# Performance work log

Hardware: AMD Instinct MI355X
Metric: run time of the kernel (lower is better)

Reference implementation:

```python
import jax, jax.numpy as jnp
import numpy as np

B, SQ, SK = 2, 2048, 2048
D, H = 1024, 16
HD = D // H              # head_dim = 64
R = 128                  # rel_pos_max_distance
P = 2 * R + 1            # num_pos_ids = 257
RADIUS = 256             # local_attention_radius


def setup_inputs() -> dict:
    key = jax.random.key(0)
    ks = jax.random.split(key, 8)
    s = 0.02
    return {
        "Q": jax.random.normal(ks[0], (B, SQ, D), dtype=jnp.float32),
        "K": jax.random.normal(ks[1], (B, SK, D), dtype=jnp.float32),
        "V": jax.random.normal(ks[2], (B, SK, D), dtype=jnp.float32),
        "Wq": jax.random.normal(ks[3], (D, D), dtype=jnp.float32) * s,
        "Wk": jax.random.normal(ks[4], (D, D), dtype=jnp.float32) * s,
        "Wv": jax.random.normal(ks[5], (D, D), dtype=jnp.float32) * s,
        "Wo": jax.random.normal(ks[6], (D, D), dtype=jnp.float32) * s,
        "E": jax.random.normal(ks[7], (P, D), dtype=jnp.float32) * s,  # rel_embeds
    }


def _split_heads(x, W):
    # bias-free projection then split: B x S x D -> B x H x S x HD
    y = x @ W.T
    b, s, _ = y.shape
    return y.reshape(b, s, H, HD).transpose(0, 2, 1, 3)


def reference(Q, K, V, Wq, Wk, Wv, Wo, E):
    q = _split_heads(Q, Wq)  # B,H,Sq,HD
    k = _split_heads(K, Wk)  # B,H,Sk,HD
    v = _split_heads(V, Wv)  # B,H,Sk,HD

    # rel_embeds reshape matches torch: E[p] viewed as (head_dim, num_heads)
    rel = E.reshape(P, HD, H).transpose(2, 0, 1)           # H,P,HD
    Q_rel = jnp.einsum("bhqd,hpd->bhqp", q, rel)           # B,H,Sq,P

    # slided relative position ids: clip(j - i, -R, R) + R
    i = jnp.arange(SQ)[:, None]
    j = jnp.arange(SK)[None, :]
    rel_ids = jnp.clip(j - i, -R, R) + R                   # Sq,Sk
    rel_shift = jnp.take_along_axis(
        Q_rel, jnp.broadcast_to(rel_ids, (B, H, SQ, SK)), axis=3
    )                                                       # B,H,Sq,Sk

    energy = (jnp.einsum("bhqd,bhkd->bhqk", q, k) + rel_shift) / jnp.sqrt(
        jnp.float32(HD)
    )

    # local attention mask: True = masked (outside window of radius RADIUS)
    mask = jnp.abs(j - i) > RADIUS                          # Sq,Sk
    mask = mask & ~jnp.all(mask, axis=-1, keepdims=True)    # never mask full rows
    energy = jnp.where(mask[None, None], -jnp.inf, energy)

    attn = jax.nn.softmax(energy, axis=-1)                  # B,H,Sq,Sk
    out = jnp.einsum("bhqk,bhkd->bhqd", attn, v)            # B,H,Sq,HD
    # torch: view(B,H,Sq,HD).permute(0,2,3,1).flatten(2,3) -> B,Sq,(HD*H)
    out = out.transpose(0, 2, 3, 1).reshape(B, SQ, D)
    return out @ Wo.T
```

## Files before the change

### kernel.cpp

```cpp
#include <hip/hip_runtime.h>
#include <hip/hip_bf16.h>

#define BATCH 2
#define SQn 2048
#define SKn 2048
#define DMODEL 1024
#define NH 16
#define HD 64
#define NPOS 257
#define RWIN 128
#define RADIUS 256

typedef __attribute__((ext_vector_type(8))) short bf16x8;
typedef __attribute__((ext_vector_type(4))) float f32x4;

static __device__ __forceinline__ unsigned short f2bf(float f) {
    union { float f; unsigned u; } v; v.f = f;
    unsigned r = (v.u + 0x7FFFu + ((v.u >> 16) & 1u)) >> 16;
    return (unsigned short)r;
}
static __device__ __forceinline__ float bf2f(unsigned short b) {
    union { unsigned u; float f; } v; v.u = ((unsigned)b) << 16;
    return v.f;
}

static __device__ __forceinline__ void gl_lds16(const unsigned short* g, unsigned short* l) {
    __builtin_amdgcn_global_load_lds(
        (const __attribute__((address_space(1))) unsigned*)g,
        (__attribute__((address_space(3))) unsigned*)l, 16, 0, 0);
}

#define SWZ(row) (((row) ^ ((row) >> 2)) & 3)

__global__ __launch_bounds__(256) void convert_kernel(
    const float* __restrict__ Q, const float* __restrict__ K, const float* __restrict__ V,
    const float* __restrict__ Wq, const float* __restrict__ Wk, const float* __restrict__ Wv,
    const float* __restrict__ Wo,
    unsigned short* __restrict__ xb,
    unsigned short* __restrict__ wb,
    unsigned short* __restrict__ woh)
{
    int i = blockIdx.x * 256 + threadIdx.x;
    if (i < 3145728) {
        int which = i >> 20;
        int off = i & 1048575;
        const float* src = which == 0 ? Q : (which == 1 ? K : V);
        unsigned short* dst = xb + (size_t)which * 4194304;
        float4 v4 = ((const float4*)src)[off];
        ushort4 o4;
        o4.x = f2bf(v4.x); o4.y = f2bf(v4.y); o4.z = f2bf(v4.z); o4.w = f2bf(v4.w);
        ((ushort4*)dst)[off] = o4;
    } else {
        int i2 = i - 3145728;
        int which = i2 >> 18;
        int off = i2 & 262143;
        if (which < 3) {
            const float* src = which == 0 ? Wq : (which == 1 ? Wk : Wv);
            unsigned short* dst = wb + (size_t)which * 1048576;
            float4 v4 = ((const float4*)src)[off];
            ushort4 o4;
            o4.x = f2bf(v4.x); o4.y = f2bf(v4.y); o4.z = f2bf(v4.z); o4.w = f2bf(v4.w);
            ((ushort4*)dst)[off] = o4;
        } else {
            float4 v4 = ((const float4*)Wo)[off];
            int e0 = off * 4;
            int n  = e0 >> 10;
            int c0 = e0 & 1023;
            int d  = c0 >> 4;
            int h0 = c0 & 15;
            woh[((size_t)(h0 + 0) * 1024 + n) * 64 + d] = f2bf(v4.x);
            woh[((size_t)(h0 + 1) * 1024 + n) * 64 + d] = f2bf(v4.y);
            woh[((size_t)(h0 + 2) * 1024 + n) * 64 + d] = f2bf(v4.z);
            woh[((size_t)(h0 + 3) * 1024 + n) * 64 + d] = f2bf(v4.w);
        }
    }
}

__global__ __launch_bounds__(256) void mfma_gemm(
    const unsigned short* __restrict__ Xall,
    const unsigned short* __restrict__ Wall,
    unsigned short* __restrict__ Yall)
{
    __shared__ unsigned short sA[128 * 32];
    __shared__ unsigned short sB[128 * 32];
    __shared__ unsigned short sT[64 * 136];

    const int tid  = threadIdx.x;
    const int wv   = tid >> 6;
    const int lane = tid & 63;
    const int quad = lane >> 4;
    const int l15  = lane & 15;
    const int z    = blockIdx.z;
    const int m0   = blockIdx.x * 128;
    const int n0   = blockIdx.y * 128;
    const int wr   = (wv >> 1) * 64;
    const int wc   = (wv & 1) * 64;

    const unsigned short* X = Xall + (size_t)z * (4096 * 1024);
    const unsigned short* W = Wall + (size_t)z * (1024 * 1024);

    int aoff[4], boff[4];
#pragma unroll
    for (int t = 0; t < 4; ++t) {
        int row = wr + t * 16 + l15;
        aoff[t] = row * 32 + ((quad ^ SWZ(row)) * 8);
        int col = wc + t * 16 + l15;
        boff[t] = col * 32 + ((quad ^ SWZ(col)) * 8);
    }

    int srow[2], scg[2], sf[2];
#pragma unroll
    for (int r = 0; r < 2; ++r) {
        int f = r * 256 + tid;
        sf[r] = f;
        srow[r] = f >> 2;
        scg[r] = (f & 3) ^ SWZ(srow[r]);
    }

    f32x4 acc[4][4];
#pragma unroll
    for (int i = 0; i < 4; ++i)
#pragma unroll
        for (int j = 0; j < 4; ++j)
            acc[i][j] = (f32x4){0.f, 0.f, 0.f, 0.f};

    for (int k0 = 0; k0 < 1024; k0 += 32) {
        __syncthreads();
#pragma unroll
        for (int r = 0; r < 2; ++r) {
            gl_lds16(X + (size_t)(m0 + srow[r]) * 1024 + k0 + scg[r] * 8, &sA[sf[r] * 8]);
            gl_lds16(W + (size_t)(n0 + srow[r]) * 1024 + k0 + scg[r] * 8, &sB[sf[r] * 8]);
        }
        __syncthreads();

        bf16x8 af[4], bfr[4];
#pragma unroll
        for (int t = 0; t < 4; ++t) af[t]  = *(const bf16x8*)&sA[aoff[t]];
#pragma unroll
        for (int t = 0; t < 4; ++t) bfr[t] = *(const bf16x8*)&sB[boff[t]];
#pragma unroll
        for (int i = 0; i < 4; ++i)
#pragma unroll
            for (int j = 0; j < 4; ++j)
                acc[i][j] = __builtin_amdgcn_mfma_f32_16x16x32_bf16(af[i], bfr[j], acc[i][j], 0, 0, 0);
    }

    unsigned short* Y = Yall + (size_t)z * (4096 * 1024);
    const int b_ = m0 >> 11;
    const int s0 = m0 & (SQn - 1);

    if (z < 2) {
#pragma unroll
        for (int i = 0; i < 4; ++i) {
            int mbase = s0 + wr + i * 16 + quad * 4;
#pragma unroll
            for (int j = 0; j < 4; ++j) {
                int col = n0 + wc + j * 16 + l15;
                int h = col >> 6, dd = col & 63;
                unsigned short* yb = Y + (((size_t)(b_ * NH + h) * SQn) << 6) + dd;
#pragma unroll
                for (int r = 0; r < 4; ++r)
                    yb[(size_t)(mbase + r) << 6] = f2bf(acc[i][j][r]);
            }
        }
    } else {
#pragma unroll
        for (int hh = 0; hh < 2; ++hh) {
            __syncthreads();
            if ((wv & 1) == hh) {
#pragma unroll
                for (int i = 0; i < 4; ++i) {
                    int mloc = wr + i * 16 + quad * 4;
#pragma unroll
                    for (int j = 0; j < 4; ++j) {
                        ushort4 pk;
                        pk.x = f2bf(acc[i][j][0]);
                        pk.y = f2bf(acc[i][j][1]);
                        pk.z = f2bf(acc[i][j][2]);
                        pk.w = f2bf(acc[i][j][3]);
                        *(ushort4*)&sT[(j * 16 + l15) * 136 + mloc] = pk;
                    }
                }
            }
            __syncthreads();
            int h = (n0 >> 6) + hh;
            unsigned short* yb = Y + ((size_t)(b_ * NH + h) * HD) * SKn + s0;
#pragma unroll
            for (int it = 0; it < 4; ++it) {
                int u = it * 256 + tid;
                int dd = u >> 4, mc = u & 15;
                uint4 val = *(const uint4*)&sT[dd * 136 + mc * 8];
                *(uint4*)(yb + (size_t)dd * SKn + mc * 8) = val;
            }
        }
    }
}

__global__ __launch_bounds__(256) void gemm_out(
    const unsigned short* __restrict__ aoh,
    const unsigned short* __restrict__ woh,
    float* __restrict__ Y)
{
    __shared__ unsigned short sA[64 * 32];
    __shared__ unsigned short sB[128 * 32];

    const int tid  = threadIdx.x;
    const int wv   = tid >> 6;
    const int lane = tid & 63;
    const int quad = lane >> 4;
    const int l15  = lane & 15;
    const int m0   = blockIdx.x * 64;
    const int n0   = blockIdx.y * 128;
    const int wr   = (wv >> 1) * 32;
    const int wc   = (wv & 1) * 64;
    const int b_   = m0 >> 11;
    const int s0   = m0 & (SQn - 1);

    int aoff[2], boff[4];
#pragma unroll
    for (int i = 0; i < 2; ++i) {
        int row = wr + i * 16 + l15;
        aoff[i] = row * 32 + ((quad ^ SWZ(row)) * 8);
    }
#pragma unroll
    for (int j = 0; j < 4; ++j) {
        int col = wc + j * 16 + l15;
        boff[j] = col * 32 + ((quad ^ SWZ(col)) * 8);
    }

    const int arow = tid >> 2;
    const int acs  = (tid & 3) ^ SWZ(arow);
    int bf_[2], brow[2], bcs[2];
#pragma unroll
    for (int r = 0; r < 2; ++r) {
        int f = r * 256 + tid;
        bf_[r] = f; brow[r] = f >> 2; bcs[r] = (f & 3) ^ SWZ(brow[r]);
    }

    f32x4 acc[2][4];
#pragma unroll
    for (int i = 0; i < 2; ++i)
#pragma unroll
        for (int j = 0; j < 4; ++j)
            acc[i][j] = (f32x4){0.f, 0.f, 0.f, 0.f};

    for (int h = 0; h < NH; ++h) {
        const unsigned short* Ah = aoh + ((size_t)(b_ * NH + h) * SQn + s0) * HD;
        const unsigned short* Bh = woh + ((size_t)h * 1024 + n0) * HD;
#pragma unroll
        for (int k0 = 0; k0 < 64; k0 += 32) {
            __syncthreads();
            gl_lds16(Ah + (size_t)arow * HD + k0 + acs * 8, &sA[tid * 8]);
#pragma unroll
            for (int r = 0; r < 2; ++r)
                gl_lds16(Bh + (size_t)brow[r] * HD + k0 + bcs[r] * 8, &sB[bf_[r] * 8]);
            __syncthreads();

            bf16x8 af[2], bfr[4];
#pragma unroll
            for (int i = 0; i < 2; ++i) af[i]  = *(const bf16x8*)&sA[aoff[i]];
#pragma unroll
            for (int j = 0; j < 4; ++j) bfr[j] = *(const bf16x8*)&sB[boff[j]];
#pragma unroll
            for (int i = 0; i < 2; ++i)
#pragma unroll
                for (int j = 0; j < 4; ++j)
                    acc[i][j] = __builtin_amdgcn_mfma_f32_16x16x32_bf16(af[i], bfr[j], acc[i][j], 0, 0, 0);
        }
    }

#pragma unroll
    for (int i = 0; i < 2; ++i) {
        int mbase = m0 + wr + i * 16 + quad * 4;
#pragma unroll
        for (int j = 0; j < 4; ++j) {
            int col = n0 + wc + j * 16 + l15;
#pragma unroll
            for (int r = 0; r < 4; ++r)
                Y[(size_t)(mbase + r) * DMODEL + col] = acc[i][j][r];
        }
    }
}

__global__ __launch_bounds__(256) void relt_kernel(
    const float* __restrict__ E, unsigned short* __restrict__ relTb)
{
    int idx = blockIdx.x * 256 + threadIdx.x;
    const int total = NH * NPOS * HD;
    if (idx < total) {
        int d = idx & (HD - 1);
        int p = (idx >> 6) % NPOS;
        int h = idx / (NPOS * HD);
        relTb[idx] = f2bf(E[(size_t)p * DMODEL + d * NH + h]);
    }
}

#define BIAS_S 9.765625e-4f

__global__ __launch_bounds__(256, 4) void attn_mfma(
    const unsigned short* __restrict__ q,
    const unsigned short* __restrict__ k,
    const unsigned short* __restrict__ vT,
    const unsigned short* __restrict__ relTb,
    unsigned short* __restrict__ aoh)
{
    __shared__ unsigned short sK[64 * 64];
    __shared__ unsigned short sP[4][16 * 72];
    __shared__ signed char    sq8[64 * 260];
    unsigned short* const sQ = (unsigned short*)sq8;

    const int tid  = threadIdx.x;
    const int w    = tid >> 6;
    const int lane = tid & 63;
    const int quad = lane >> 4;
    const int l15  = lane & 15;
    const int xcd  = blockIdx.x & 7;
    const int sidx = blockIdx.x >> 3;
    const int bh   = (xcd << 2) | (sidx >> 5);
    const int q0   = (sidx & 31) << 6;
    const int h    = bh & (NH - 1);

    const int f1 = tid,       row1 = f1 >> 3;
    const int c1 = ((f1 & 7) ^ (row1 & 7)) * 8;
    const int f2 = 256 + tid, row2 = f2 >> 3;
    const int c2 = ((f2 & 7) ^ (row2 & 7)) * 8;

    {
        const unsigned short* gq = q + ((size_t)bh * SQn + q0) * HD;
        gl_lds16(gq + row1 * HD + c1, &sQ[f1 * 8]);
        gl_lds16(gq + row2 * HD + c2, &sQ[f2 * 8]);
    }
    __syncthreads();

    const int qrow = w * 16 + l15;
    const int qs = (quad ^ (qrow & 7)) * 8;
    bf16x8 a0 = *(const bf16x8*)&sQ[qrow * 64 + qs];
    bf16x8 a1 = *(const bf16x8*)&sQ[qrow * 64 + (qs ^ 32)];

    const int myrow = w * 16 + quad * 4;
    for (int c5 = 0; c5 < 5; ++c5) {
        __syncthreads();
        const unsigned short* gr = relTb + ((size_t)h * NPOS + c5 * 64) * HD;
        gl_lds16(gr + row1 * HD + c1, &sK[f1 * 8]);
        gl_lds16(gr + row2 * HD + c2, &sK[f2 * 8]);
        __syncthreads();
#pragma unroll
        for (int t = 0; t < 4; ++t) {
            int prow = t * 16 + l15;
            int ks = (quad ^ (prow & 7)) * 8;
            bf16x8 b0 = *(const bf16x8*)&sK[prow * 64 + ks];
            bf16x8 b1 = *(const bf16x8*)&sK[prow * 64 + (ks ^ 32)];
            f32x4 cc = {0.f, 0.f, 0.f, 0.f};
            cc = __builtin_amdgcn_mfma_f32_16x16x32_bf16(a0, b0, cc, 0, 0, 0);
            cc = __builtin_amdgcn_mfma_f32_16x16x32_bf16(a1, b1, cc, 0, 0, 0);
            int pos = c5 * 64 + t * 16 + l15;
            if (pos < NPOS) {
#pragma unroll
                for (int r = 0; r < 4; ++r) {
                    int iq = (int)rintf(cc[r] * 128.0f);
                    iq = iq < -127 ? -127 : (iq > 127 ? 127 : iq);
                    sq8[(myrow + r) * 260 + pos] = (signed char)iq;
                }
            }
        }
    }
    __syncthreads();

    float bias0[4], bias256[4];
#pragma unroll
    for (int r = 0; r < 4; ++r) {
        bias0[r]   = (float)sq8[(myrow + r) * 260 + 0]   * BIAS_S;
        bias256[r] = (float)sq8[(myrow + r) * 260 + 256] * BIAS_S;
    }

    const int lo = (q0 - RADIUS) > 0 ? (q0 - RADIUS) : 0;
    const int hi = (q0 + 63 + RADIUS) < (SKn - 1) ? (q0 + 63 + RADIUS) : (SKn - 1);
    const int nt = ((hi - lo) >> 6) + 1;
    const int e_ = l15 - quad * 4;

    const unsigned short* kg = k  + (size_t)bh * SKn * HD;
    const unsigned short* vg = vT + (size_t)bh * HD * SKn;

    float lacc[4] = {0.f, 0.f, 0.f, 0.f};
    f32x4 o[4];
#pragma unroll
    for (int t = 0; t < 4; ++t) o[t] = (f32x4){0.f, 0.f, 0.f, 0.f};

    {
        gl_lds16(kg + (size_t)(lo + row1) * HD + c1, &sK[f1 * 8]);
        gl_lds16(kg + (size_t)(lo + row2) * HD + c2, &sK[f2 * 8]);
    }

    for (int kt = 0; kt < nt; ++kt) {
        const int kb = lo + (kt << 6);
        __syncthreads();

        bf16x8 kf0[4], kf1[4];
#pragma unroll
        for (int t = 0; t < 4; ++t) {
            int prow = t * 16 + l15;
            int ks = (quad ^ (prow & 7)) * 8;
            kf0[t] = *(const bf16x8*)&sK[prow * 64 + ks];
            kf1[t] = *(const bf16x8*)&sK[prow * 64 + (ks ^ 32)];
        }
        __syncthreads();

        if (kt + 1 < nt) {
            const int kb2 = kb + 64;
            gl_lds16(kg + (size_t)(kb2 + row1) * HD + c1, &sK[f1 * 8]);
            gl_lds16(kg + (size_t)(kb2 + row2) * HD + c2, &sK[f2 * 8]);
        }

        bf16x8 vf0[4], vf1[4];
#pragma unroll
        for (int t = 0; t < 4; ++t) {
            const unsigned short* vrow = vg + (size_t)(t * 16 + l15) * SKn + kb;
            vf0[t] = *(const bf16x8*)(vrow + quad * 8);
            vf1[t] = *(const bf16x8*)(vrow + 32 + quad * 8);
        }

        const int dtbase = kb - q0 - w * 16;
#pragma unroll
        for (int t = 0; t < 4; ++t) {
            const int dt = dtbase + t * 16;
            const int spb = (quad * 4) * 72 + t * 16 + l15;
            if (dt <= -272 || dt >= 272) {
#pragma unroll
                for (int r = 0; r < 4; ++r) sP[w][spb + r * 72] = 0;
            } else {
                f32x4 sc = {0.f, 0.f, 0.f, 0.f};
                sc = __builtin_amdgcn_mfma_f32_16x16x32_bf16(a0, kf0[t], sc, 0, 0, 0);
                sc = __builtin_amdgcn_mfma_f32_16x16x32_bf16(a1, kf1[t], sc, 0, 0, 0);

                float pv[4];
                if (dt >= -112 && dt <= 112) {
                    int idx0 = myrow * 260 + dt + 128 + e_;
#pragma unroll
                    for (int r = 0; r < 4; ++r) {
                        float bf = (float)sq8[idx0 + r * 259] * BIAS_S;
                        pv[r] = __expf(fmaf(sc[r], 0.125f, bf));
                    }
                } else if (dt >= -240 && dt <= -144) {
#pragma unroll
                    for (int r = 0; r < 4; ++r)
                        pv[r] = __expf(fmaf(sc[r], 0.125f, bias0[r]));
                } else if (dt >= 144 && dt <= 240) {
#pragma unroll
                    for (int r = 0; r < 4; ++r)
                        pv[r] = __expf(fmaf(sc[r], 0.125f, bias256[r]));
                } else {
#pragma unroll
                    for (int r = 0; r < 4; ++r) {
                        int d = dt + e_ - r;
                        bool in = (unsigned)(d + RADIUS) <= 2u * RADIUS;
                        int p = d < -RWIN ? 0 : (d > RWIN ? 2 * RWIN : d + RWIN);
                        float bf = (float)sq8[(myrow + r) * 260 + p] * BIAS_S;
                        float e = __expf(fmaf(sc[r], 0.125f, bf));
                        pv[r] = in ? e : 0.0f;
                    }
                }
#pragma unroll
                for (int r = 0; r < 4; ++r) {
                    unsigned short pb = f2bf(pv[r]);
                    sP[w][spb + r * 72] = pb;
                    lacc[r] += bf2f(pb);
                }
            }
        }

        bf16x8 p0 = *(const bf16x8*)&sP[w][l15 * 72 + quad * 8];
        bf16x8 p1 = *(const bf16x8*)&sP[w][l15 * 72 + 32 + quad * 8];
#pragma unroll
        for (int t = 0; t < 4; ++t) {
            o[t] = __builtin_amdgcn_mfma_f32_16x16x32_bf16(p0, vf0[t], o[t], 0, 0, 0);
            o[t] = __builtin_amdgcn_mfma_f32_16x16x32_bf16(p1, vf1[t], o[t], 0, 0, 0);
        }
    }

    float linv[4];
#pragma unroll
    for (int r = 0; r < 4; ++r) {
        float l = lacc[r];
#pragma unroll
        for (int off = 1; off <= 8; off <<= 1) l += __shfl_xor(l, off);
        linv[r] = 1.0f / l;
    }

    unsigned short* ob = aoh + ((size_t)bh * SQn + q0) * HD;
#pragma unroll
    for (int t = 0; t < 4; ++t) {
#pragma unroll
        for (int r = 0; r < 4; ++r) {
            int irow = w * 16 + quad * 4 + r;
            ob[irow * HD + t * 16 + l15] = f2bf(o[t][r] * linv[r]);
        }
    }
}

extern "C" void kernel_launch(void* const* d_in, const int* in_sizes, int n_in,
                              void* d_out, int out_size, void* d_ws, size_t ws_size,
                              hipStream_t stream) {
    const float* Q  = (const float*)d_in[0];
    const float* K  = (const float*)d_in[1];
    const float* V  = (const float*)d_in[2];
    const float* Wq = (const float*)d_in[3];
    const float* Wk = (const float*)d_in[4];
    const float* Wv = (const float*)d_in[5];
    const float* Wo = (const float*)d_in[6];
    const float* E  = (const float*)d_in[7];
    float* out = (float*)d_out;

    char* p = (char*)d_ws;
    unsigned short* xb    = (unsigned short*)p; p += (size_t)24 << 20;
    unsigned short* wb    = (unsigned short*)p; p += (size_t)6  << 20;
    unsigned short* woh   = (unsigned short*)p; p += (size_t)2  << 20;
    unsigned short* head  = (unsigned short*)p; p += (size_t)24 << 20;
    unsigned short* relTb = (unsigned short*)p; p += (size_t)1  << 20;
    unsigned short* aoh   = (unsigned short*)p;

    unsigned short* qb  = head;
    unsigned short* kb  = head + 4194304;
    unsigned short* vTb = head + 8388608;

    dim3 bb(256);
    convert_kernel<<<dim3(16384), bb, 0, stream>>>(Q, K, V, Wq, Wk, Wv, Wo, xb, wb, woh);
    relt_kernel<<<dim3(1028), bb, 0, stream>>>(E, relTb);
    mfma_gemm<<<dim3(32, 8, 3), bb, 0, stream>>>(xb, wb, head);
    attn_mfma<<<dim3(BATCH * NH * (SQn / 64)), bb, 0, stream>>>(qb, kb, vTb, relTb, aoh);
    gemm_out<<<dim3(64, 8), bb, 0, stream>>>(aoh, woh, out);
}
```

Measured before the change: 217.7 us.

## Register-prefetch K/V tiles, transpose score MFMA, use exp2 and packed bf16 convert

Removes the LDS staging of K and the two block-wide barriers per key tile. Each wave now loads K and V fragments straight from global memory into registers one tile ahead, so the next tile's loads overlap the current tile's compute. The score MFMA swaps its operands so each lane owns one query row. That turns the bias lookups into contiguous reads and lets the row-sum be a single scalar reduced with fewer shuffles. It also folds log2(e) into the scale constants to use native exp2, and packs P with v_cvt_pk_bf16 into 64-bit LDS stores, at the cost of more registers and redundant global K reads across waves.

```diff
diff --git a/kernel.cpp b/kernel.cpp
--- a/kernel.cpp
+++ b/kernel.cpp
@@ -19,9 +19,11 @@
     unsigned r = (v.u + 0x7FFFu + ((v.u >> 16) & 1u)) >> 16;
     return (unsigned short)r;
 }
-static __device__ __forceinline__ float bf2f(unsigned short b) {
-    union { unsigned u; float f; } v; v.u = ((unsigned)b) << 16;
-    return v.f;
+
+static __device__ __forceinline__ unsigned cvt_pk_bf16(float lo, float hi) {
+    unsigned r;
+    asm("v_cvt_pk_bf16_f32 %0, %1, %2" : "=v"(r) : "v"(lo), "v"(hi));
+    return r;
 }
 
 static __device__ __forceinline__ void gl_lds16(const unsigned short* g, unsigned short* l) {
@@ -295,7 +297,8 @@
     }
 }
 
-#define BIAS_S 9.765625e-4f
+#define BIAS_S2 0.0014089565402528222f
+#define SC2     0.1803368801111204f
 
 __global__ __launch_bounds__(256, 4) void attn_mfma(
     const unsigned short* __restrict__ q,
@@ -366,105 +369,91 @@
     }
     __syncthreads();
 
-    float bias0[4], bias256[4];
-#pragma unroll
-    for (int r = 0; r < 4; ++r) {
-        bias0[r]   = (float)sq8[(myrow + r) * 260 + 0]   * BIAS_S;
-        bias256[r] = (float)sq8[(myrow + r) * 260 + 256] * BIAS_S;
-    }
+    const int qr = w * 16 + l15;
+    const int e2 = quad * 4 - l15;
+    const float bias0   = (float)sq8[qr * 260 + 0]   * BIAS_S2;
+    const float bias256 = (float)sq8[qr * 260 + 256] * BIAS_S2;
 
     const int lo = (q0 - RADIUS) > 0 ? (q0 - RADIUS) : 0;
     const int hi = (q0 + 63 + RADIUS) < (SKn - 1) ? (q0 + 63 + RADIUS) : (SKn - 1);
     const int nt = ((hi - lo) >> 6) + 1;
-    const int e_ = l15 - quad * 4;
 
     const unsigned short* kg = k  + (size_t)bh * SKn * HD;
     const unsigned short* vg = vT + (size_t)bh * HD * SKn;
 
-    float lacc[4] = {0.f, 0.f, 0.f, 0.f};
+    float lacc = 0.f;
     f32x4 o[4];
 #pragma unroll
     for (int t = 0; t < 4; ++t) o[t] = (f32x4){0.f, 0.f, 0.f, 0.f};
 
-    {
-        gl_lds16(kg + (size_t)(lo + row1) * HD + c1, &sK[f1 * 8]);
-        gl_lds16(kg + (size_t)(lo + row2) * HD + c2, &sK[f2 * 8]);
+    bf16x8 kc0[4], kc1[4], vf0[4], vf1[4];
+#pragma unroll
+    for (int t = 0; t < 4; ++t) {
+        const unsigned short* krow = kg + (size_t)(lo + t * 16 + l15) * HD;
+        kc0[t] = *(const bf16x8*)(krow + quad * 8);
+        kc1[t] = *(const bf16x8*)(krow + 32 + quad * 8);
+    }
+#pragma unroll
+    for (int t = 0; t < 4; ++t) {
+        const unsigned short* vrow = vg + (size_t)(t * 16 + l15) * SKn + lo;
+        vf0[t] = *(const bf16x8*)(vrow + quad * 8);
+        vf1[t] = *(const bf16x8*)(vrow + 32 + quad * 8);
     }
 
     for (int kt = 0; kt < nt; ++kt) {
-        const int kb = lo + (kt << 6);
-        __syncthreads();
-
-        bf16x8 kf0[4], kf1[4];
+        const int kb  = lo + (kt << 6);
+        const int kb2 = (kt + 1 < nt) ? kb + 64 : kb;
+        const int dtbase = kb - q0 - w * 16;
+
 #pragma unroll
         for (int t = 0; t < 4; ++t) {
-            int prow = t * 16 + l15;
-            int ks = (quad ^ (prow & 7)) * 8;
-            kf0[t] = *(const bf16x8*)&sK[prow * 64 + ks];
-            kf1[t] = *(const bf16x8*)&sK[prow * 64 + (ks ^ 32)];
-        }
-        __syncthreads();
-
-        if (kt + 1 < nt) {
-            const int kb2 = kb + 64;
-            gl_lds16(kg + (size_t)(kb2 + row1) * HD + c1, &sK[f1 * 8]);
-            gl_lds16(kg + (size_t)(kb2 + row2) * HD + c2, &sK[f2 * 8]);
-        }
-
-        bf16x8 vf0[4], vf1[4];
-#pragma unroll
-        for (int t = 0; t < 4; ++t) {
-            const unsigned short* vrow = vg + (size_t)(t * 16 + l15) * SKn + kb;
-            vf0[t] = *(const bf16x8*)(vrow + quad * 8);
-            vf1[t] = *(const bf16x8*)(vrow + 32 + quad * 8);
-        }
-
-        const int dtbase = kb - q0 - w * 16;
-#pragma unroll
-        for (int t = 0; t < 4; ++t) {
-            const int dt = dtbase + t * 16;
-            const int spb = (quad * 4) * 72 + t * 16 + l15;
+            const int dt  = dtbase + t * 16;
+            const int spw = l15 * 72 + t * 16 + quad * 4;
+            const unsigned short* krow = kg + (size_t)(kb2 + t * 16 + l15) * HD;
             if (dt <= -272 || dt >= 272) {
-#pragma unroll
-                for (int r = 0; r < 4; ++r) sP[w][spb + r * 72] = 0;
+                kc0[t] = *(const bf16x8*)(krow + quad * 8);
+                kc1[t] = *(const bf16x8*)(krow + 32 + quad * 8);
+                *(uint2*)&sP[w][spw] = (uint2){0u, 0u};
             } else {
                 f32x4 sc = {0.f, 0.f, 0.f, 0.f};
-                sc = __builtin_amdgcn_mfma_f32_16x16x32_bf16(a0, kf0[t], sc, 0, 0, 0);
-                sc = __builtin_amdgcn_mfma_f32_16x16x32_bf16(a1, kf1[t], sc, 0, 0, 0);
+                sc = __builtin_amdgcn_mfma_f32_16x16x32_bf16(kc0[t], a0, sc, 0, 0, 0);
+                sc = __builtin_amdgcn_mfma_f32_16x16x32_bf16(kc1[t], a1, sc, 0, 0, 0);
+                kc0[t] = *(const bf16x8*)(krow + quad * 8);
+                kc1[t] = *(const bf16x8*)(krow + 32 + quad * 8);
 
                 float pv[4];
                 if (dt >= -112 && dt <= 112) {
-                    int idx0 = myrow * 260 + dt + 128 + e_;
+                    const int idx0 = qr * 260 + dt + e2 + 128;
+#pragma unroll
+                    for (int r = 0; r < 4; ++r)
+                        pv[r] = __builtin_amdgcn_exp2f(
+                            fmaf(sc[r], SC2, (float)sq8[idx0 + r] * BIAS_S2));
+                } else if (dt >= -240 && dt <= -144) {
+#pragma unroll
+                    for (int r = 0; r < 4; ++r)
+                        pv[r] = __builtin_amdgcn_exp2f(fmaf(sc[r], SC2, bias0));
+                } else if (dt >= 144 && dt <= 240) {
+#pragma unroll
+                    for (int r = 0; r < 4; ++r)
+                        pv[r] = __builtin_amdgcn_exp2f(fmaf(sc[r], SC2, bias256));
+                } else {
 #pragma unroll
                     for (int r = 0; r < 4; ++r) {
-                        float bf = (float)sq8[idx0 + r * 259] * BIAS_S;
-                        pv[r] = __expf(fmaf(sc[r], 0.125f, bf));
-                    }
-                } else if (dt >= -240 && dt <= -144) {
-#pragma unroll
-                    for (int r = 0; r < 4; ++r)
-                        pv[r] = __expf(fmaf(sc[r], 0.125f, bias0[r]));
-                } else if (dt >= 144 && dt <= 240) {
-#pragma unroll
-                    for (int r = 0; r < 4; ++r)
-                        pv[r] = __expf(fmaf(sc[r], 0.125f, bias256[r]));
-                } else {
-#pragma unroll
-                    for (int r = 0; r < 4; ++r) {
-                        int d = dt + e_ - r;
+                        int d = dt + e2 + r;
                         bool in = (unsigned)(d + RADIUS) <= 2u * RADIUS;
                         int p = d < -RWIN ? 0 : (d > RWIN ? 2 * RWIN : d + RWIN);
-                        float bf = (float)sq8[(myrow + r) * 260 + p] * BIAS_S;
-                        float e = __expf(fmaf(sc[r], 0.125f, bf));
+                        float bf = (float)sq8[qr * 260 + p] * BIAS_S2;
+                        float e = __builtin_amdgcn_exp2f(fmaf(sc[r], SC2, bf));
                         pv[r] = in ? e : 0.0f;
                     }
                 }
-#pragma unroll
-                for (int r = 0; r < 4; ++r) {
-                    unsigned short pb = f2bf(pv[r]);
-                    sP[w][spb + r * 72] = pb;
-                    lacc[r] += bf2f(pb);
-                }
+                unsigned pk0 = cvt_pk_bf16(pv[0], pv[1]);
+                unsigned pk1 = cvt_pk_bf16(pv[2], pv[3]);
+                *(uint2*)&sP[w][spw] = (uint2){pk0, pk1};
+                union { unsigned u; float f; } u0, u1, u2, u3;
+                u0.u = pk0 << 16; u1.u = pk0 & 0xFFFF0000u;
+                u2.u = pk1 << 16; u3.u = pk1 & 0xFFFF0000u;
+                lacc += (u0.f + u1.f) + (u2.f + u3.f);
             }
         }
 
@@ -475,16 +464,21 @@
             o[t] = __builtin_amdgcn_mfma_f32_16x16x32_bf16(p0, vf0[t], o[t], 0, 0, 0);
             o[t] = __builtin_amdgcn_mfma_f32_16x16x32_bf16(p1, vf1[t], o[t], 0, 0, 0);
         }
-    }
-
+#pragma unroll
+        for (int t = 0; t < 4; ++t) {
+            const unsigned short* vrow = vg + (size_t)(t * 16 + l15) * SKn + kb2;
+            vf0[t] = *(const bf16x8*)(vrow + quad * 8);
+            vf1[t] = *(const bf16x8*)(vrow + 32 + quad * 8);
+        }
+    }
+
+    float l = lacc;
+    l += __shfl_xor(l, 16);
+    l += __shfl_xor(l, 32);
+    float li = 1.0f / l;
     float linv[4];
 #pragma unroll
-    for (int r = 0; r < 4; ++r) {
-        float l = lacc[r];
-#pragma unroll
-        for (int off = 1; off <= 8; off <<= 1) l += __shfl_xor(l, off);
-        linv[r] = 1.0f / l;
-    }
+    for (int r = 0; r < 4; ++r) linv[r] = __shfl(li, quad * 4 + r);
 
     unsigned short* ob = aoh + ((size_t)bh * SQn + q0) * HD;
 #pragma unroll
```

Measured after the change: 243.7 us. 1.12x slower.
